# Performance work log

Measured on AMD Instinct MI355X. Metric: run time of the kernel, lower is better.

Reference implementation:

```python
import jax, jax.numpy as jnp
import numpy as np

L, H, C, V, BLK = 6, 16, 1024, 32000, 2048
B, T, TA = 2, 512, 512
DFF = 4 * C
STD = 0.02
PROJ_STD = 0.02 / np.sqrt(2 * L)  # c_proj init per module
SCALE = 1.0 / np.sqrt(C // H)


def setup_inputs() -> dict:
    key = jax.random.key(0)
    ks = iter(jax.random.split(key, 64))
    nrm = lambda shape, std=STD: jax.random.normal(next(ks), shape, jnp.float32) * std
    inp = {
        'idx': jax.random.randint(next(ks), (B, T), 0, V),
        'xa': jax.random.normal(next(ks), (B, TA, C), jnp.float32),
        'wte': nrm((V, C)),            # tied with lm_head
        'wpe': nrm((BLK, C)),
        'ln1_w': jnp.ones((L, C)), 'ln1_b': jnp.zeros((L, C)),
        'sa_wq': nrm((L, C, C)), 'sa_bq': jnp.zeros((L, C)),
        'sa_wk': nrm((L, C, C)), 'sa_bk': jnp.zeros((L, C)),
        'sa_wv': nrm((L, C, C)), 'sa_bv': jnp.zeros((L, C)),
        'sa_wo': nrm((L, C, C), PROJ_STD), 'sa_bo': jnp.zeros((L, C)),
        'ca_wq': nrm((L, C, C)), 'ca_bq': jnp.zeros((L, C)),
        'ca_wk': nrm((L, C, C)), 'ca_bk': jnp.zeros((L, C)),
        'ca_wv': nrm((L, C, C)), 'ca_bv': jnp.zeros((L, C)),
        'ca_wo': nrm((L, C, C), PROJ_STD), 'ca_bo': jnp.zeros((L, C)),
        'ln2_w': jnp.ones((L, C)), 'ln2_b': jnp.zeros((L, C)),
        'fc_w': nrm((L, C, DFF)), 'fc_b': jnp.zeros((L, DFF)),
        'pr_w': nrm((L, DFF, C), PROJ_STD), 'pr_b': jnp.zeros((L, C)),
        'lnf_w': jnp.ones((C,)), 'lnf_b': jnp.zeros((C,)),
    }
    return inp


def _ln(h, w, b):
    m = h.mean(-1, keepdims=True)
    v = jnp.mean((h - m) ** 2, -1, keepdims=True)
    return (h - m) * jax.lax.rsqrt(v + 1e-5) * w + b


def _gelu(h):  # new_gelu (tanh approximation)
    return 0.5 * h * (1.0 + jnp.tanh(np.sqrt(2.0 / np.pi) * (h + 0.044715 * h ** 3)))


def _attn(hq, hkv, wq, bq, wk, bk, wv, bv, wo, bo):
    # NB: the original applies a tril causal mask even for cross-attention.
    Bq, Tq, _ = hq.shape
    Tk = hkv.shape[1]
    D = C // H
    q = (hq @ wq + bq).reshape(Bq, Tq, H, D)
    k = (hkv @ wk + bk).reshape(Bq, Tk, H, D)
    v = (hkv @ wv + bv).reshape(Bq, Tk, H, D)
    att = jnp.einsum('bqhd,bkhd->bhqk', q, k) * SCALE
    mask = jnp.tril(jnp.ones((Tq, Tk), bool))
    att = jnp.where(mask, att, -jnp.inf)
    att = jax.nn.softmax(att, axis=-1)
    y = jnp.einsum('bhqk,bkhd->bqhd', att, v).reshape(Bq, Tq, C)
    return y @ wo + bo


def _forward(idx, xa, wte, wpe, ln1_w, ln1_b, sa_wq, sa_bq, sa_wk, sa_bk, sa_wv, sa_bv, sa_wo, sa_bo,
             ca_wq, ca_bq, ca_wk, ca_bk, ca_wv, ca_bv, ca_wo, ca_bo,
             ln2_w, ln2_b, fc_w, fc_b, pr_w, pr_b, lnf_w, lnf_b):
    t = idx.shape[1]
    x = wte[idx] + wpe[:t][None]  # [B,T,C]

    def block(h, p):
        (l1w, l1b, sqw, sqb, skw, skb, svw, svb, sow, sob,
         cqw, cqb, ckw, ckb, cvw, cvb, cow, cob,
         l2w, l2b, fw, fb, pw, pb) = p
        n = _ln(h, l1w, l1b)
        h = h + _attn(n, n, sqw, sqb, skw, skb, svw, svb, sow, sob)
        n = _ln(h, l1w, l1b)  # ln_1 reused for cross-attn, as in source
        h = h + _attn(n, xa, cqw, cqb, ckw, ckb, cvw, cvb, cow, cob)
        n = _ln(h, l2w, l2b)
        h = h + (_gelu(n @ fw + fb) @ pw + pb)
        return h, None

    xs = (ln1_w, ln1_b, sa_wq, sa_bq, sa_wk, sa_bk, sa_wv, sa_bv, sa_wo, sa_bo,
          ca_wq, ca_bq, ca_wk, ca_bk, ca_wv, ca_bv, ca_wo, ca_bo,
          ln2_w, ln2_b, fc_w, fc_b, pr_w, pr_b)
    x, _ = jax.lax.scan(block, x, xs)
    x = _ln(x, lnf_w, lnf_b)
    return x @ wte.T  # tied lm_head, [B,T,V]


def reference(idx, xa, wte, wpe, ln1_w, ln1_b, sa_wq, sa_bq, sa_wk, sa_bk, sa_wv, sa_bv, sa_wo, sa_bo,
              ca_wq, ca_bq, ca_wk, ca_bk, ca_wv, ca_bv, ca_wo, ca_bo,
              ln2_w, ln2_b, fc_w, fc_b, pr_w, pr_b, lnf_w, lnf_b):
    return _forward(idx, xa, wte, wpe, ln1_w, ln1_b, sa_wq, sa_bq, sa_wk, sa_bk, sa_wv, sa_bv, sa_wo, sa_bo,
                    ca_wq, ca_bq, ca_wk, ca_bk, ca_wv, ca_bv, ca_wo, ca_bo,
                    ln2_w, ln2_b, fc_w, fc_b, pr_w, pr_b, lnf_w, lnf_b)
```

## Files before the change

### kernel.cpp

```cpp
#include <hip/hip_runtime.h>
#include <math.h>

#define CC   1024
#define HH   16
#define DH   64
#define TT   512
#define NTOK 1024
#define DFF_ 4096
#define VV   32000
#define QKSCALE 0.125f

typedef unsigned short u16;
typedef __attribute__((ext_vector_type(8))) short short8;
typedef __attribute__((ext_vector_type(4))) float f32x4;

__device__ __forceinline__ u16 f2bf(float f) {
  union { float f; unsigned u; } v; v.f = f;
  unsigned r = v.u + 0x7FFFu + ((v.u >> 16) & 1u);
  return (u16)(r >> 16);
}
__device__ __forceinline__ float gelu_f(float h) {
  return 0.5f * h * (1.0f + tanhf(0.7978845608028654f * (h + 0.044715f * h * h * h)));
}

#define GLD16(gp, lp) __builtin_amdgcn_global_load_lds( \
    (const __attribute__((address_space(1))) void*)(gp), \
    (__attribute__((address_space(3))) void*)(lp), 16, 0, 0)

#define MFMA(a, b, c) __builtin_amdgcn_mfma_f32_16x16x32_bf16(a, b, c, 0, 0, 0)

__global__ __launch_bounds__(256) void embed_kernel(
    const int* __restrict__ idx, const float* __restrict__ wte,
    const float* __restrict__ wpe, float* __restrict__ x) {
  int row = blockIdx.x;
  int t = row & (TT - 1);
  int id = idx[row];
  const float4* a = (const float4*)(wte + (size_t)id * CC);
  const float4* p = (const float4*)(wpe + (size_t)t * CC);
  float4* o = (float4*)(x + (size_t)row * CC);
  int c = threadIdx.x;
  float4 va = a[c], vp = p[c];
  float4 ov;
  ov.x = va.x + vp.x; ov.y = va.y + vp.y; ov.z = va.z + vp.z; ov.w = va.w + vp.w;
  o[c] = ov;
}

__global__ __launch_bounds__(256) void ln_kernel(
    const float* __restrict__ x, const float* __restrict__ w,
    const float* __restrict__ b, u16* __restrict__ out) {
  int row = blockIdx.x, tid = threadIdx.x;
  float4 v = ((const float4*)(x + (size_t)row * CC))[tid];
  float s  = v.x + v.y + v.z + v.w;
  float sq = fmaf(v.x, v.x, fmaf(v.y, v.y, fmaf(v.z, v.z, v.w * v.w)));
  for (int o = 32; o > 0; o >>= 1) { s += __shfl_down(s, o); sq += __shfl_down(sq, o); }
  __shared__ float rs[4], rq[4];
  int wid = tid >> 6, lane = tid & 63;
  if (lane == 0) { rs[wid] = s; rq[wid] = sq; }
  __syncthreads();
  s  = rs[0] + rs[1] + rs[2] + rs[3];
  sq = rq[0] + rq[1] + rq[2] + rq[3];
  float mean = s * (1.0f / CC);
  float var  = sq * (1.0f / CC) - mean * mean;
  float rstd = 1.0f / sqrtf(var + 1e-5f);
  float4 wv = ((const float4*)w)[tid];
  float4 bv = ((const float4*)b)[tid];
  ushort4 o;
  o.x = f2bf((v.x - mean) * rstd * wv.x + bv.x);
  o.y = f2bf((v.y - mean) * rstd * wv.y + bv.y);
  o.z = f2bf((v.z - mean) * rstd * wv.z + bv.z);
  o.w = f2bf((v.w - mean) * rstd * wv.w + bv.w);
  ((ushort4*)(out + (size_t)row * CC))[tid] = o;
}

__global__ __launch_bounds__(256) void wtrans16_kernel(
    const float* __restrict__ w0, const float* __restrict__ w1,
    const float* __restrict__ w2, const float* __restrict__ w3,
    const float* __restrict__ w4, const float* __restrict__ w5,
    const float* __restrict__ w6, const float* __restrict__ w7,
    const float* __restrict__ fc, const float* __restrict__ pr,
    u16* __restrict__ wt) {
  const size_t M1 = 1048576;
  int z = blockIdx.z;
  const float* src;
  size_t doff;
  int sstr, dstr;
  if (z < 8) {
    src = z == 0 ? w0 : z == 1 ? w1 : z == 2 ? w2 : z == 3 ? w3
        : z == 4 ? w4 : z == 5 ? w5 : z == 6 ? w6 : w7;
    sstr = 1024; doff = (size_t)z * M1; dstr = 1024;
  } else if (z < 12) {
    int s = z - 8;
    src = fc + (size_t)s * 1024; sstr = 4096;
    doff = 8 * M1 + (size_t)s * M1; dstr = 1024;
  } else {
    int s = z - 12;
    src = pr + (size_t)s * M1; sstr = 1024;
    doff = 12 * M1 + (size_t)s * 1024; dstr = 4096;
  }
  __shared__ float t[32][33];
  int bx = blockIdx.x * 32, by = blockIdx.y * 32;
  int c = threadIdx.x & 31, r = threadIdx.x >> 5;
#pragma unroll
  for (int i = 0; i < 4; ++i)
    t[r + i * 8][c] = src[(size_t)(by + r + i * 8) * sstr + bx + c];
  __syncthreads();
#pragma unroll
  for (int i = 0; i < 4; ++i)
    wt[doff + (size_t)(bx + r + i * 8) * dstr + by + c] = f2bf(t[c][r + i * 8]);
}

__global__ __launch_bounds__(256) void convbf_kernel(
    const float* __restrict__ in, u16* __restrict__ out, int n4) {
  int i = blockIdx.x * 256 + threadIdx.x;
  if (i < n4) {
    float4 v = ((const float4*)in)[i];
    ushort4 o; o.x = f2bf(v.x); o.y = f2bf(v.y); o.z = f2bf(v.z); o.w = f2bf(v.w);
    ((ushort4*)out)[i] = o;
  }
}

template <int EPI, int MODE, int BM, int BN>
__global__ __launch_bounds__(256) void gemm_bf16_kernel(
    const u16* __restrict__ A, const u16* __restrict__ B,
    const float* __restrict__ bias, const float* __restrict__ bias2,
    const float* __restrict__ bias3, float* __restrict__ Cm,
    int K, int ldc, int whichbase) {
  constexpr int WM = BM / 2, WN = BN / 2, MF = WM / 16, NF = WN / 16;
  constexpr int PA = BM / 32, PB = BN / 32;
  __shared__ u16 As[BM * 64];
  __shared__ u16 Bs[BN * 64];
  int tid = threadIdx.x;
  int lane = tid & 63, wave = tid >> 6;
  int wr = wave >> 1, wc = wave & 1;
  int row0, col0;
  if (MODE == 2) {
    int id = blockIdx.x;
    int wg = (id & 7) * 250 + (id >> 3);
    row0 = (wg & 7) * BM;
    col0 = (wg >> 3) * BN;
  } else {
    row0 = blockIdx.y * BM;
    col0 = blockIdx.x * BN;
  }
  f32x4 acc[MF][NF];
#pragma unroll
  for (int m = 0; m < MF; ++m)
#pragma unroll
    for (int n = 0; n < NF; ++n) acc[m][n] = (f32x4){0.f, 0.f, 0.f, 0.f};

  int srow = tid >> 3;
  int sblk = (tid & 7) ^ ((tid >> 3) & 7);
  const u16* Ab = A + (size_t)row0 * K;
  const u16* Bb = B + (size_t)col0 * K;
  int arow = wr * WM + (lane & 15);
  int brow = wc * WN + (lane & 15);
  int g8 = lane >> 4;

  for (int k0 = 0; k0 < K; k0 += 64) {
#pragma unroll
    for (int p = 0; p < PA; ++p)
      GLD16(Ab + (size_t)(p * 32 + srow) * K + k0 + sblk * 8,
            &As[p * 2048 + wave * 512]);
#pragma unroll
    for (int p = 0; p < PB; ++p)
      GLD16(Bb + (size_t)(p * 32 + srow) * K + k0 + sblk * 8,
            &Bs[p * 2048 + wave * 512]);
    __syncthreads();
#pragma unroll
    for (int ks = 0; ks < 2; ++ks) {
      short8 af[MF], bg[NF];
#pragma unroll
      for (int m = 0; m < MF; ++m) {
        int row = arow + m * 16;
        af[m] = *(const short8*)&As[row * 64 + (((ks * 4 + g8) ^ (row & 7)) << 3)];
      }
#pragma unroll
      for (int n = 0; n < NF; ++n) {
        int row = brow + n * 16;
        bg[n] = *(const short8*)&Bs[row * 64 + (((ks * 4 + g8) ^ (row & 7)) << 3)];
      }
#pragma unroll
      for (int m = 0; m < MF; ++m)
#pragma unroll
        for (int n = 0; n < NF; ++n)
          acc[m][n] = MFMA(af[m], bg[n], acc[m][n]);
    }
    __syncthreads();
  }

  int r0 = row0 + wr * WM + g8 * 4;
  int c0 = col0 + wc * WN + (lane & 15);

  if (EPI == 4) {
    u16* qb = (u16*)Cm;
#pragma unroll
    for (int m = 0; m < MF; ++m)
#pragma unroll
      for (int n = 0; n < NF; ++n) {
        int j = c0 + n * 16;
        int which = whichbase + (j >> 10);
        const float* bp = (j >> 10) == 0 ? bias : ((j >> 10) == 1 ? bias2 : bias3);
        float bj = bp ? bp[j & 1023] : 0.0f;
        int h = (j & 1023) >> 6, d = j & 63;
        int trow0 = r0 + m * 16;
        int b = trow0 >> 9, t0 = trow0 & 511;
        int bh = b * 16 + h;
        u16 vals[4];
#pragma unroll
        for (int r = 0; r < 4; ++r) vals[r] = f2bf(acc[m][n][r] + bj);
        if (which < 2) {
          u16* dst = qb + (size_t)which * 1048576 + (size_t)bh * 32768 + (size_t)t0 * 64 + d;
#pragma unroll
          for (int r = 0; r < 4; ++r) dst[(size_t)r * 64] = vals[r];
        } else {
          u16* dst = qb + 2 * 1048576 + (size_t)bh * 32768 + (size_t)d * 512 + t0;
          *(ushort4*)dst = *(ushort4*)vals;
        }
      }
    return;
  }

  float bj[NF];
#pragma unroll
  for (int n = 0; n < NF; ++n)
    bj[n] = bias ? bias[c0 + n * 16] : 0.0f;
  u16* Cb = (u16*)Cm;
#pragma unroll
  for (int m = 0; m < MF; ++m)
#pragma unroll
    for (int n = 0; n < NF; ++n)
#pragma unroll
      for (int r = 0; r < 4; ++r) {
        size_t off = (size_t)(r0 + m * 16 + r) * ldc + c0 + n * 16;
        float v = acc[m][n][r] + bj[n];
        if (EPI == 0) Cm[off] = v;
        else if (EPI == 1) Cm[off] += v;
        else if (EPI == 2) Cb[off] = f2bf(gelu_f(v));
      }
}

__global__ __launch_bounds__(256) void attn_kernel(
    const u16* __restrict__ qh, const u16* __restrict__ kh,
    const u16* __restrict__ vt, u16* __restrict__ y) {
  __shared__ u16 P[32 * 512];
  __shared__ float smax[4][32], ssum[4][32];
  int tid = threadIdx.x, lane = tid & 63, w = tid >> 6;
  int bx = blockIdx.x, bh = blockIdx.y;
  int q0 = bx * 32;
  int b = bh >> 4, h = bh & 15;
  const u16* qb = qh + (size_t)bh * 32768;
  const u16* kb = kh + (size_t)bh * 32768;
  const u16* vb = vt + (size_t)bh * 32768;
  int g = lane >> 4, c = lane & 15;

  short8 a[2][2];
#pragma unroll
  for (int rt = 0; rt < 2; ++rt)
#pragma unroll
    for (int ks = 0; ks < 2; ++ks)
      a[rt][ks] = *(const short8*)(qb + (size_t)(q0 + rt * 16 + c) * 64 + ks * 32 + g * 8);

  int lim = q0 + 31;
  int nct = (lim - w * 128) / 16 + 1;
  if (nct > 8) nct = 8;
  if (nct < 0) nct = 0;
  f32x4 s[2][8];
#pragma unroll
  for (int rt = 0; rt < 2; ++rt)
#pragma unroll
    for (int ct = 0; ct < 8; ++ct) s[rt][ct] = (f32x4){0.f, 0.f, 0.f, 0.f};
  for (int ct = 0; ct < nct; ++ct) {
    int n0 = w * 128 + ct * 16;
#pragma unroll
    for (int ks = 0; ks < 2; ++ks) {
      short8 bf = *(const short8*)(kb + (size_t)(n0 + c) * 64 + ks * 32 + g * 8);
      s[0][ct] = MFMA(a[0][ks], bf, s[0][ct]);
      s[1][ct] = MFMA(a[1][ks], bf, s[1][ct]);
    }
  }

  float mx[2][4];
#pragma unroll
  for (int rt = 0; rt < 2; ++rt)
#pragma unroll
    for (int r = 0; r < 4; ++r) mx[rt][r] = -1e30f;
  for (int ct = 0; ct < nct; ++ct) {
    int col = w * 128 + ct * 16 + c;
#pragma unroll
    for (int rt = 0; rt < 2; ++rt)
#pragma unroll
      for (int r = 0; r < 4; ++r) {
        int trow = q0 + rt * 16 + g * 4 + r;
        float v = s[rt][ct][r] * QKSCALE;
        if (col > trow) v = -1e30f;
        s[rt][ct][r] = v;
        mx[rt][r] = fmaxf(mx[rt][r], v);
      }
  }
#pragma unroll
  for (int off = 1; off < 16; off <<= 1)
#pragma unroll
    for (int rt = 0; rt < 2; ++rt)
#pragma unroll
      for (int r = 0; r < 4; ++r) mx[rt][r] = fmaxf(mx[rt][r], __shfl_xor(mx[rt][r], off));
  if (c == 0)
#pragma unroll
    for (int rt = 0; rt < 2; ++rt)
#pragma unroll
      for (int r = 0; r < 4; ++r) smax[w][rt * 16 + g * 4 + r] = mx[rt][r];
  __syncthreads();

  float m_[2][4], sum[2][4];
#pragma unroll
  for (int rt = 0; rt < 2; ++rt)
#pragma unroll
    for (int r = 0; r < 4; ++r) {
      int row = rt * 16 + g * 4 + r;
      m_[rt][r] = fmaxf(fmaxf(smax[0][row], smax[1][row]), fmaxf(smax[2][row], smax[3][row]));
      sum[rt][r] = 0.f;
    }
  for (int ct = 0; ct < nct; ++ct) {
    int col = w * 128 + ct * 16 + c;
    int blk = col >> 3, cl = col & 7;
#pragma unroll
    for (int rt = 0; rt < 2; ++rt)
#pragma unroll
      for (int r = 0; r < 4; ++r) {
        float p = __expf(s[rt][ct][r] - m_[rt][r]);
        sum[rt][r] += p;
        int row = rt * 16 + g * 4 + r;
        int hsh = (row ^ (row >> 2)) & 7;
        P[row * 512 + ((blk ^ hsh) << 3) + cl] = f2bf(p);
      }
  }
#pragma unroll
  for (int off = 1; off < 16; off <<= 1)
#pragma unroll
    for (int rt = 0; rt < 2; ++rt)
#pragma unroll
      for (int r = 0; r < 4; ++r) sum[rt][r] += __shfl_xor(sum[rt][r], off);
  if (c == 0)
#pragma unroll
    for (int rt = 0; rt < 2; ++rt)
#pragma unroll
      for (int r = 0; r < 4; ++r) ssum[w][rt * 16 + g * 4 + r] = sum[rt][r];
  __syncthreads();

  float li[2][4];
#pragma unroll
  for (int rt = 0; rt < 2; ++rt)
#pragma unroll
    for (int r = 0; r < 4; ++r) {
      int row = rt * 16 + g * 4 + r;
      li[rt][r] = 1.0f / (ssum[0][row] + ssum[1][row] + ssum[2][row] + ssum[3][row]);
    }

  int rt2 = w >> 1, nh = w & 1;
  f32x4 o[2];
  o[0] = (f32x4){0.f, 0.f, 0.f, 0.f};
  o[1] = (f32x4){0.f, 0.f, 0.f, 0.f};
  int nks = bx + 1;
  int prow = rt2 * 16 + c;
  int phsh = (prow ^ (prow >> 2)) & 7;
  for (int ks = 0; ks < nks; ++ks) {
    short8 pa = *(const short8*)&P[prow * 512 + (((ks * 4 + g) ^ phsh) << 3)];
#pragma unroll
    for (int nt = 0; nt < 2; ++nt) {
      int d = nh * 32 + nt * 16 + c;
      short8 vf = *(const short8*)(vb + (size_t)d * 512 + ks * 32 + g * 8);
      o[nt] = MFMA(pa, vf, o[nt]);
    }
  }
#pragma unroll
  for (int nt = 0; nt < 2; ++nt)
#pragma unroll
    for (int r = 0; r < 4; ++r) {
      int trow = q0 + rt2 * 16 + g * 4 + r;
      float val = o[nt][r] * li[rt2][r];
      y[(size_t)(b * 512 + trow) * 1024 + h * 64 + nh * 32 + nt * 16 + c] = f2bf(val);
    }
}

extern "C" void kernel_launch(void* const* d_in, const int* in_sizes, int n_in,
                              void* d_out, int out_size, void* d_ws, size_t ws_size,
                              hipStream_t stream) {
  const int*   idx   = (const int*)d_in[0];
  const float* xa    = (const float*)d_in[1];
  const float* wte   = (const float*)d_in[2];
  const float* wpe   = (const float*)d_in[3];
  const float* ln1_w = (const float*)d_in[4];
  const float* ln1_b = (const float*)d_in[5];
  const float* sa_wq = (const float*)d_in[6];
  const float* sa_bq = (const float*)d_in[7];
  const float* sa_wk = (const float*)d_in[8];
  const float* sa_bk = (const float*)d_in[9];
  const float* sa_wv = (const float*)d_in[10];
  const float* sa_bv = (const float*)d_in[11];
  const float* sa_wo = (const float*)d_in[12];
  const float* sa_bo = (const float*)d_in[13];
  const float* ca_wq = (const float*)d_in[14];
  const float* ca_bq = (const float*)d_in[15];
  const float* ca_wk = (const float*)d_in[16];
  const float* ca_bk = (const float*)d_in[17];
  const float* ca_wv = (const float*)d_in[18];
  const float* ca_bv = (const float*)d_in[19];
  const float* ca_wo = (const float*)d_in[20];
  const float* ca_bo = (const float*)d_in[21];
  const float* ln2_w = (const float*)d_in[22];
  const float* ln2_b = (const float*)d_in[23];
  const float* fc_w  = (const float*)d_in[24];
  const float* fc_b  = (const float*)d_in[25];
  const float* pr_w  = (const float*)d_in[26];
  const float* pr_b  = (const float*)d_in[27];
  const float* lnf_w = (const float*)d_in[28];
  const float* lnf_b = (const float*)d_in[29];

  const size_t M1 = 1048576;
  float* ws     = (float*)d_ws;
  float* x      = ws;
  u16* qkvh  = (u16*)(x + M1);
  u16* nbf   = qkvh + 3 * M1;
  u16* ybf   = nbf + M1;
  u16* hmbf  = ybf + M1;
  u16* xabf  = hmbf + 4 * M1;
  u16* wtebf = xabf + M1;
  u16* wT    = wtebf + (size_t)VV * CC;

  const size_t oQKV = 0, oWO = 3 * M1, oCQ = 4 * M1, oCKV = 5 * M1,
               oCWO = 7 * M1, oFC = 8 * M1, oPR = 12 * M1;

  embed_kernel<<<NTOK, 256, 0, stream>>>(idx, wte, wpe, x);
  convbf_kernel<<<(VV * CC / 4 + 255) / 256, 256, 0, stream>>>(wte, wtebf, VV * CC / 4);
  convbf_kernel<<<(NTOK * CC / 4 + 255) / 256, 256, 0, stream>>>(xa, xabf, NTOK * CC / 4);

  for (int l = 0; l < 6; ++l) {
    size_t wofs = (size_t)l * CC * CC;
    size_t bofs = (size_t)l * CC;
    size_t mofs = (size_t)l * CC * DFF_;

    wtrans16_kernel<<<dim3(32, 32, 16), 256, 0, stream>>>(
        sa_wq + wofs, sa_wk + wofs, sa_wv + wofs, sa_wo + wofs,
        ca_wq + wofs, ca_wk + wofs, ca_wv + wofs, ca_wo + wofs,
        fc_w + mofs, pr_w + mofs, wT);

    ln_kernel<<<NTOK, 256, 0, stream>>>(x, ln1_w + bofs, ln1_b + bofs, nbf);
    gemm_bf16_kernel<4, 0, 64, 128><<<dim3(24, 16), 256, 0, stream>>>(
        nbf, wT + oQKV, sa_bq + bofs, sa_bk + bofs, sa_bv + bofs,
        (float*)qkvh, CC, 0, 0);
    attn_kernel<<<dim3(16, 32), 256, 0, stream>>>(qkvh, qkvh + M1, qkvh + 2 * M1, ybf);
    gemm_bf16_kernel<1, 0, 64, 64><<<dim3(16, 16), 256, 0, stream>>>(
        ybf, wT + oWO, sa_bo + bofs, nullptr, nullptr, x, CC, CC, 0);

    ln_kernel<<<NTOK, 256, 0, stream>>>(x, ln1_w + bofs, ln1_b + bofs, nbf);
    gemm_bf16_kernel<4, 0, 64, 64><<<dim3(16, 16), 256, 0, stream>>>(
        nbf, wT + oCQ, ca_bq + bofs, nullptr, nullptr, (float*)qkvh, CC, 0, 0);
    gemm_bf16_kernel<4, 0, 64, 128><<<dim3(16, 16), 256, 0, stream>>>(
        xabf, wT + oCKV, ca_bk + bofs, ca_bv + bofs, nullptr,
        (float*)qkvh, CC, 0, 1);
    attn_kernel<<<dim3(16, 32), 256, 0, stream>>>(qkvh, qkvh + M1, qkvh + 2 * M1, ybf);
    gemm_bf16_kernel<1, 0, 64, 64><<<dim3(16, 16), 256, 0, stream>>>(
        ybf, wT + oCWO, ca_bo + bofs, nullptr, nullptr, x, CC, CC, 0);

    ln_kernel<<<NTOK, 256, 0, stream>>>(x, ln2_w + bofs, ln2_b + bofs, nbf);
    gemm_bf16_kernel<2, 0, 128, 128><<<dim3(32, 8), 256, 0, stream>>>(
        nbf, wT + oFC, fc_b + (size_t)l * DFF_, nullptr, nullptr,
        (float*)hmbf, CC, DFF_, 0);
    gemm_bf16_kernel<1, 0, 64, 64><<<dim3(16, 16), 256, 0, stream>>>(
        hmbf, wT + oPR, pr_b + bofs, nullptr, nullptr, x, DFF_, CC, 0);
  }

  ln_kernel<<<NTOK, 256, 0, stream>>>(x, lnf_w, lnf_b, nbf);
  gemm_bf16_kernel<0, 2, 128, 128><<<dim3(2000), 256, 0, stream>>>(
      nbf, wtebf, nullptr, nullptr, nullptr, (float*)d_out, CC, VV, 0);
}
```

Before: 1.668 ms.

## Double-buffer LDS tiles in bf16 GEMM with configurable BK and MFMA priority

```diff
diff --git a/kernel.cpp b/kernel.cpp
--- a/kernel.cpp
+++ b/kernel.cpp
@@ -119,16 +119,20 @@
   }
 }
 
-template <int EPI, int MODE, int BM, int BN>
+template <int EPI, int MODE, int BM, int BN, int BK>
 __global__ __launch_bounds__(256) void gemm_bf16_kernel(
     const u16* __restrict__ A, const u16* __restrict__ B,
     const float* __restrict__ bias, const float* __restrict__ bias2,
     const float* __restrict__ bias3, float* __restrict__ Cm,
     int K, int ldc, int whichbase) {
   constexpr int WM = BM / 2, WN = BN / 2, MF = WM / 16, NF = WN / 16;
-  constexpr int PA = BM / 32, PB = BN / 32;
-  __shared__ u16 As[BM * 64];
-  __shared__ u16 Bs[BN * 64];
+  constexpr int KS = BK / 32;
+  constexpr int NB = BK / 8;
+  constexpr int PA = BM * BK / 2048;
+  constexpr int PB = BN * BK / 2048;
+  constexpr int RPP = 2048 / BK;
+  __shared__ u16 As[2][BM * BK];
+  __shared__ u16 Bs[2][BN * BK];
   int tid = threadIdx.x;
   int lane = tid & 63, wave = tid >> 6;
   int wr = wave >> 1, wc = wave & 1;
@@ -148,42 +152,58 @@
 #pragma unroll
     for (int n = 0; n < NF; ++n) acc[m][n] = (f32x4){0.f, 0.f, 0.f, 0.f};
 
-  int srow = tid >> 3;
-  int sblk = (tid & 7) ^ ((tid >> 3) & 7);
+  int srow = tid / NB;
+  int sblk = (BK == 64) ? ((tid & 7) ^ ((tid >> 3) & 7))
+                        : ((tid & 3) ^ ((tid >> 3) & 3));
   const u16* Ab = A + (size_t)row0 * K;
   const u16* Bb = B + (size_t)col0 * K;
   int arow = wr * WM + (lane & 15);
   int brow = wc * WN + (lane & 15);
   int g8 = lane >> 4;
 
-  for (int k0 = 0; k0 < K; k0 += 64) {
+  auto stage = [&](int bufi, int k0) {
 #pragma unroll
     for (int p = 0; p < PA; ++p)
-      GLD16(Ab + (size_t)(p * 32 + srow) * K + k0 + sblk * 8,
-            &As[p * 2048 + wave * 512]);
+      GLD16(Ab + (size_t)(p * RPP + srow) * K + k0 + sblk * 8,
+            &As[bufi][p * 2048 + wave * 512]);
 #pragma unroll
     for (int p = 0; p < PB; ++p)
-      GLD16(Bb + (size_t)(p * 32 + srow) * K + k0 + sblk * 8,
-            &Bs[p * 2048 + wave * 512]);
-    __syncthreads();
-#pragma unroll
-    for (int ks = 0; ks < 2; ++ks) {
+      GLD16(Bb + (size_t)(p * RPP + srow) * K + k0 + sblk * 8,
+            &Bs[bufi][p * 2048 + wave * 512]);
+  };
+
+  const int NT = K / BK;
+  stage(0, 0);
+  __syncthreads();
+  for (int t = 0; t < NT; ++t) {
+    int cur = t & 1;
+    if (t + 1 < NT) stage(cur ^ 1, (t + 1) * BK);
+    const u16* Ac = As[cur];
+    const u16* Bc = Bs[cur];
+#pragma unroll
+    for (int ks = 0; ks < KS; ++ks) {
       short8 af[MF], bg[NF];
 #pragma unroll
       for (int m = 0; m < MF; ++m) {
         int row = arow + m * 16;
-        af[m] = *(const short8*)&As[row * 64 + (((ks * 4 + g8) ^ (row & 7)) << 3)];
+        int off = (BK == 64) ? row * 64 + (((ks * 4 + g8) ^ (row & 7)) << 3)
+                             : row * 32 + ((g8 ^ ((row >> 1) & 3)) << 3);
+        af[m] = *(const short8*)&Ac[off];
       }
 #pragma unroll
       for (int n = 0; n < NF; ++n) {
         int row = brow + n * 16;
-        bg[n] = *(const short8*)&Bs[row * 64 + (((ks * 4 + g8) ^ (row & 7)) << 3)];
-      }
+        int off = (BK == 64) ? row * 64 + (((ks * 4 + g8) ^ (row & 7)) << 3)
+                             : row * 32 + ((g8 ^ ((row >> 1) & 3)) << 3);
+        bg[n] = *(const short8*)&Bc[off];
+      }
+      __builtin_amdgcn_s_setprio(1);
 #pragma unroll
       for (int m = 0; m < MF; ++m)
 #pragma unroll
         for (int n = 0; n < NF; ++n)
           acc[m][n] = MFMA(af[m], bg[n], acc[m][n]);
+      __builtin_amdgcn_s_setprio(0);
     }
     __syncthreads();
   }
@@ -444,32 +464,32 @@
         fc_w + mofs, pr_w + mofs, wT);
 
     ln_kernel<<<NTOK, 256, 0, stream>>>(x, ln1_w + bofs, ln1_b + bofs, nbf);
-    gemm_bf16_kernel<4, 0, 64, 128><<<dim3(24, 16), 256, 0, stream>>>(
+    gemm_bf16_kernel<4, 0, 64, 128, 64><<<dim3(24, 16), 256, 0, stream>>>(
         nbf, wT + oQKV, sa_bq + bofs, sa_bk + bofs, sa_bv + bofs,
         (float*)qkvh, CC, 0, 0);
     attn_kernel<<<dim3(16, 32), 256, 0, stream>>>(qkvh, qkvh + M1, qkvh + 2 * M1, ybf);
-    gemm_bf16_kernel<1, 0, 64, 64><<<dim3(16, 16), 256, 0, stream>>>(
+    gemm_bf16_kernel<1, 0, 64, 64, 64><<<dim3(16, 16), 256, 0, stream>>>(
         ybf, wT + oWO, sa_bo + bofs, nullptr, nullptr, x, CC, CC, 0);
 
     ln_kernel<<<NTOK, 256, 0, stream>>>(x, ln1_w + bofs, ln1_b + bofs, nbf);
-    gemm_bf16_kernel<4, 0, 64, 64><<<dim3(16, 16), 256, 0, stream>>>(
+    gemm_bf16_kernel<4, 0, 64, 64, 64><<<dim3(16, 16), 256, 0, stream>>>(
         nbf, wT + oCQ, ca_bq + bofs, nullptr, nullptr, (float*)qkvh, CC, 0, 0);
-    gemm_bf16_kernel<4, 0, 64, 128><<<dim3(16, 16), 256, 0, stream>>>(
+    gemm_bf16_kernel<4, 0, 64, 128, 64><<<dim3(16, 16), 256, 0, stream>>>(
         xabf, wT + oCKV, ca_bk + bofs, ca_bv + bofs, nullptr,
         (float*)qkvh, CC, 0, 1);
     attn_kernel<<<dim3(16, 32), 256, 0, stream>>>(qkvh, qkvh + M1, qkvh + 2 * M1, ybf);
-    gemm_bf16_kernel<1, 0, 64, 64><<<dim3(16, 16), 256, 0, stream>>>(
+    gemm_bf16_kernel<1, 0, 64, 64, 64><<<dim3(16, 16), 256, 0, stream>>>(
         ybf, wT + oCWO, ca_bo + bofs, nullptr, nullptr, x, CC, CC, 0);
 
     ln_kernel<<<NTOK, 256, 0, stream>>>(x, ln2_w + bofs, ln2_b + bofs, nbf);
-    gemm_bf16_kernel<2, 0, 128, 128><<<dim3(32, 8), 256, 0, stream>>>(
+    gemm_bf16_kernel<2, 0, 128, 128, 32><<<dim3(32, 8), 256, 0, stream>>>(
         nbf, wT + oFC, fc_b + (size_t)l * DFF_, nullptr, nullptr,
         (float*)hmbf, CC, DFF_, 0);
-    gemm_bf16_kernel<1, 0, 64, 64><<<dim3(16, 16), 256, 0, stream>>>(
+    gemm_bf16_kernel<1, 0, 64, 64, 64><<<dim3(16, 16), 256, 0, stream>>>(
         hmbf, wT + oPR, pr_b + bofs, nullptr, nullptr, x, DFF_, CC, 0);
   }
 
   ln_kernel<<<NTOK, 256, 0, stream>>>(x, lnf_w, lnf_b, nbf);
-  gemm_bf16_kernel<0, 2, 128, 128><<<dim3(2000), 256, 0, stream>>>(
+  gemm_bf16_kernel<0, 2, 128, 128, 32><<<dim3(2000), 256, 0, stream>>>(
       nbf, wtebf, nullptr, nullptr, nullptr, (float*)d_out, CC, VV, 0);
 }
```

New measurement: 1.670 ms. About the same (+0.1%).
